# Kernel tuning notes

Hardware: AMD Instinct MI355X
Metric: run time of the kernel (lower is better)

The kernel has to match this reference:

```python
import jax, jax.numpy as jnp
import numpy as np

N = 100000   # nodes
E = 220000   # directed edges (each branch)
H = 128      # hidden_dim
OUT = 1      # output_dim
G = 4096     # num graphs in batch
PE = 5       # laplacian eigenvector PE dims
VOCAB = 28   # atom types


def gcn_conv(x, src, dst, W, b, n):
    # PyG GCNConv: x' = D^-1/2 (A + I) D^-1/2 (X W) + b
    h = x @ W
    deg = jax.ops.segment_sum(jnp.ones(src.shape[0], x.dtype), dst, num_segments=n) + 1.0
    dinv = jax.lax.rsqrt(deg)
    coef = dinv[src] * dinv[dst]                                    # [E]
    agg = jax.ops.segment_sum(h[src] * coef[:, None], dst, num_segments=n)
    agg = agg + h * (dinv * dinv)[:, None]                          # self-loop term
    return agg + b


def gcn2(x, edge_index, W1, b1, W2, b2, n):
    # PyG GCN model, num_layers=2: conv -> relu -> conv
    src, dst = edge_index[0], edge_index[1]
    h = jax.nn.relu(gcn_conv(x, src, dst, W1, b1, n))
    return gcn_conv(h, src, dst, W2, b2, n)


def setup_inputs() -> dict:
    key = jax.random.key(0)
    ks = jax.random.split(key, 16)
    s = 0.1
    return {
        "node_tokens": jax.random.randint(ks[0], (N, 1), 0, VOCAB),
        "pe": jax.random.normal(ks[1], (N, PE), jnp.float32),
        "edge_index": jax.random.randint(ks[2], (2, E), 0, N),
        "vr_edge_index": jax.random.randint(ks[3], (2, E), 0, N),
        "batch": jnp.sort(jax.random.randint(ks[4], (N,), 0, G)),
        "embed_table": jax.random.normal(ks[5], (VOCAB, H), jnp.float32) * s,
        "Wt": jax.random.normal(ks[6], (PE, H), jnp.float32) * s,
        "bt": jnp.zeros((H,), jnp.float32),
        "W1": jax.random.normal(ks[7], (H, H), jnp.float32) * s,
        "b1": jnp.zeros((H,), jnp.float32),
        "W2": jax.random.normal(ks[8], (H, OUT), jnp.float32) * s,
        "b2": jnp.zeros((OUT,), jnp.float32),
        "Wv1": jax.random.normal(ks[9], (H, H), jnp.float32) * s,
        "bv1": jnp.zeros((H,), jnp.float32),
        "Wv2": jax.random.normal(ks[10], (H, OUT), jnp.float32) * s,
        "bv2": jnp.zeros((OUT,), jnp.float32),
    }


def reference(node_tokens, pe, edge_index, vr_edge_index, batch, embed_table,
              Wt, bt, W1, b1, W2, b2, Wv1, bv1, Wv2, bv2):
    # embed_x(data.x.long()).squeeze(1) + lin_trans(pe)
    x = embed_table[node_tokens[:, 0]] + (pe @ Wt + bt)             # [N, H]
    x1 = gcn2(x, edge_index, W1, b1, W2, b2, N)                     # [N, OUT]
    xv = gcn2(x, vr_edge_index, Wv1, bv1, Wv2, bv2, N)              # [N, OUT]
    x1 = x1 + xv
    y_hat = jax.ops.segment_sum(x1, batch, num_segments=G)          # [G, OUT]
    y_hat = jnp.squeeze(y_hat, axis=-1)                             # [G]
    return (y_hat, x)
```

## Files before the change

### kernel.cpp

```cpp
#include <hip/hip_runtime.h>

#define NN 100000
#define NE 220000
#define HD 128
#define NG 4096
#define NPE 5
#define NB_SCAN ((NN + 255) / 256)
#define NBF ((NN + 127) / 128)
#define NBW 128
#define NBZ ((2 * NN + 255) / 256)
#define NBD ((2 * NE + 255) / 256)
#define LDP 136

typedef unsigned int uint;
typedef unsigned short ushort;
typedef __attribute__((ext_vector_type(8))) short bf16x8;
typedef __attribute__((ext_vector_type(4))) float f32x4;

__device__ __forceinline__ float bf2f(uint u16) {
    return __uint_as_float(u16 << 16);
}
__device__ __forceinline__ ushort f2bf(float f) {
    uint u = __float_as_uint(f);
    u += 0x7fffu + ((u >> 16) & 1u);
    return (ushort)(u >> 16);
}

__global__ void k_prep0(const float* __restrict__ W1, const float* __restrict__ Wv1,
                        ushort* __restrict__ Wcat, int* __restrict__ cnt) {
    int b = blockIdx.x;
    if (b < NBW) {
        int t = b * 256 + threadIdx.x;
        int f = t >> 7, k = t & 127;
        const float* W = (f < HD) ? W1 : Wv1;
        Wcat[t] = f2bf(W[k * HD + (f & 127)]);
    } else {
        int t = (b - NBW) * 256 + threadIdx.x;
        if (t < 2 * NN) cnt[t] = 0;
    }
}

__global__ __launch_bounds__(256) void k_front_gemm(
        const int* __restrict__ tok, const float* __restrict__ pe,
        const float* __restrict__ embed, const float* __restrict__ Wtr,
        const float* __restrict__ bt, float* __restrict__ x,
        const ushort* __restrict__ Wcat, ushort* __restrict__ H,
        const int* __restrict__ ei, const int* __restrict__ vei,
        int* __restrict__ cnt) {
    __shared__ ushort As[128 * LDP];
    int b = blockIdx.x;
    if (b < NBF) {
        int tid = threadIdx.x;
        int n0 = b * 128;
        int q = tid & 31;
        int nlb = tid >> 5;
        for (int r = 0; r < 16; ++r) {
            int nl = r * 8 + nlb;
            int n = n0 + nl;
            uint2 pk = {0u, 0u};
            if (n < NN) {
                int t = tok[n];
                float4 acc = ((const float4*)(embed + (size_t)t * HD))[q];
                float4 bv = ((const float4*)bt)[q];
                acc.x += bv.x; acc.y += bv.y; acc.z += bv.z; acc.w += bv.w;
                const float* pen = pe + n * NPE;
#pragma unroll
                for (int k = 0; k < NPE; ++k) {
                    float p = pen[k];
                    float4 wv = ((const float4*)(Wtr + k * HD))[q];
                    acc.x += p * wv.x; acc.y += p * wv.y;
                    acc.z += p * wv.z; acc.w += p * wv.w;
                }
                ((float4*)x)[n * 32 + q] = acc;
                pk.x = (uint)f2bf(acc.x) | ((uint)f2bf(acc.y) << 16);
                pk.y = (uint)f2bf(acc.z) | ((uint)f2bf(acc.w) << 16);
            }
            *(uint2*)&As[nl * LDP + q * 4] = pk;
        }
        __syncthreads();
        int w = tid >> 6, lane = tid & 63;
        int m = lane & 15, quad = lane >> 4;
#pragma unroll
        for (int fh = 0; fh < 2; ++fh) {
            const ushort* Wg = Wcat + (size_t)fh * 128 * 128;
            f32x4 acc[2][8] = {};
#pragma unroll
            for (int kc = 0; kc < 4; ++kc) {
                int k0 = kc * 32 + quad * 8;
                bf16x8 xf[2];
#pragma unroll
                for (int nt = 0; nt < 2; ++nt)
                    xf[nt] = *(const bf16x8*)&As[((w * 2 + nt) * 16 + m) * LDP + k0];
#pragma unroll
                for (int ft = 0; ft < 8; ++ft) {
                    bf16x8 wf = *(const bf16x8*)&Wg[(ft * 16 + m) * 128 + k0];
#pragma unroll
                    for (int nt = 0; nt < 2; ++nt)
                        acc[nt][ft] = __builtin_amdgcn_mfma_f32_16x16x32_bf16(
                            wf, xf[nt], acc[nt][ft], 0, 0, 0);
                }
            }
#pragma unroll
            for (int nt = 0; nt < 2; ++nt) {
                int n = n0 + (w * 2 + nt) * 16 + m;
                if (n >= NN) continue;
#pragma unroll
                for (int ft = 0; ft < 8; ++ft) {
                    f32x4 a = acc[nt][ft];
                    uint2 pk;
                    pk.x = (uint)f2bf(a[0]) | ((uint)f2bf(a[1]) << 16);
                    pk.y = (uint)f2bf(a[2]) | ((uint)f2bf(a[3]) << 16);
                    *(uint2*)&H[(size_t)n * 256 + fh * 128 + ft * 16 + quad * 4] = pk;
                }
            }
        }
    } else {
        int t = (b - NBF) * 256 + threadIdx.x;
        if (t < 2 * NE) {
            int br = t >= NE;
            int e = t - br * NE;
            const int* S = br ? vei : ei;
            atomicAdd(&cnt[br * NN + S[NE + e]], 1);
        }
    }
}

__global__ void k_scan1(const int* __restrict__ cnt, int* __restrict__ off,
                        int* __restrict__ bsum, float* __restrict__ dinv,
                        float* __restrict__ y) {
    __shared__ int s[256];
    int tid = threadIdx.x;
    int gid = blockIdx.x * 256 + tid;
    if (gid < NG) y[gid] = 0.f;
    int br = blockIdx.x / NB_SCAN;
    int blk = blockIdx.x % NB_SCAN;
    int i = blk * 256 + tid;
    int v = (i < NN) ? cnt[br * NN + i] : 0;
    if (i < NN) dinv[br * NN + i] = rsqrtf((float)v + 1.0f);
    s[tid] = v;
    __syncthreads();
    for (int d = 1; d < 256; d <<= 1) {
        int t = (tid >= d) ? s[tid - d] : 0;
        __syncthreads();
        s[tid] += t;
        __syncthreads();
    }
    if (i < NN) off[br * NN + i] = s[tid] - v;
    if (tid == 255) bsum[br * 512 + blk] = s[255];
}

__global__ void k_scan2(int* __restrict__ bsum) {
    __shared__ int s[512];
    int br = blockIdx.x;
    int tid = threadIdx.x;
    int v = (tid < NB_SCAN) ? bsum[br * 512 + tid] : 0;
    s[tid] = v;
    __syncthreads();
    for (int d = 1; d < 512; d <<= 1) {
        int t = (tid >= d) ? s[tid - d] : 0;
        __syncthreads();
        s[tid] += t;
        __syncthreads();
    }
    if (tid < NB_SCAN) bsum[br * 512 + tid] = s[tid] - v;
}

__global__ void k_scan3(const int* __restrict__ off, const int* __restrict__ bsum,
                        const int* __restrict__ cnt, int2* __restrict__ off2,
                        int* __restrict__ cur) {
    int br = blockIdx.x / NB_SCAN;
    int blk = blockIdx.x % NB_SCAN;
    int i = blk * 256 + threadIdx.x;
    if (i < NN) {
        int o = off[br * NN + i] + bsum[br * 512 + blk];
        int2 pr;
        pr.x = o;
        pr.y = o + cnt[br * NN + i];
        off2[br * NN + i] = pr;
        cur[br * NN + i] = o;
    }
}

__global__ void k_scatter(const int* __restrict__ ei, const int* __restrict__ vei,
                          const float* __restrict__ dinv, int* __restrict__ cur,
                          int2* __restrict__ ent) {
    int t = blockIdx.x * blockDim.x + threadIdx.x;
    if (t >= 2 * NE) return;
    int br = t >= NE;
    int e = t - br * NE;
    const int* S = br ? vei : ei;
    int s = S[e], d = S[NE + e];
    int pos = atomicAdd(&cur[br * NN + d], 1);
    int2 rec;
    rec.x = s;
    rec.y = __float_as_int(dinv[br * NN + s] * dinv[br * NN + d]);
    ent[br * NE + pos] = rec;
}

__global__ void k_gather_ep(const ushort* __restrict__ H, const float* __restrict__ dinv,
                            const int2* __restrict__ off2,
                            const int2* __restrict__ ent,
                            const float* __restrict__ b1, const float* __restrict__ bv1,
                            const float* __restrict__ W2, const float* __restrict__ Wv2,
                            float* __restrict__ z) {
    int wid = threadIdx.x >> 6;
    int lane = threadIdx.x & 63;
    int half = lane >> 5;
    int l = lane & 31;
    int task = blockIdx.x * 8 + wid * 2 + half;
    int br = task >= NN;
    int n = task - br * NN;

    const int2* en = ent + br * NE;
    size_t hoff = (size_t)br * 128;

    float dv = dinv[br * NN + n];
    uint2 u = *(const uint2*)(H + (size_t)n * 256 + hoff + l * 4);
    float c = dv * dv;
    float a0 = bf2f(u.x & 0xffffu) * c, a1 = bf2f(u.x >> 16) * c;
    float a2 = bf2f(u.y & 0xffffu) * c, a3 = bf2f(u.y >> 16) * c;

    int2 pr = off2[br * NN + n];
    int p0 = pr.x, p1 = pr.y;
    for (int p = p0; p < p1; p += 4) {
        int2 e0 = en[p], e1 = en[p + 1], e2 = en[p + 2], e3 = en[p + 3];
        int s0 = e0.x;
        int s1 = (p + 1 < p1) ? e1.x : n;
        int s2 = (p + 2 < p1) ? e2.x : n;
        int s3 = (p + 3 < p1) ? e3.x : n;
        float c0 = __int_as_float(e0.y);
        float c1 = (p + 1 < p1) ? __int_as_float(e1.y) : 0.f;
        float c2 = (p + 2 < p1) ? __int_as_float(e2.y) : 0.f;
        float c3 = (p + 3 < p1) ? __int_as_float(e3.y) : 0.f;
        uint2 v0 = *(const uint2*)(H + (size_t)s0 * 256 + hoff + l * 4);
        uint2 v1 = *(const uint2*)(H + (size_t)s1 * 256 + hoff + l * 4);
        uint2 v2 = *(const uint2*)(H + (size_t)s2 * 256 + hoff + l * 4);
        uint2 v3 = *(const uint2*)(H + (size_t)s3 * 256 + hoff + l * 4);
        a0 += bf2f(v0.x & 0xffffu) * c0; a1 += bf2f(v0.x >> 16) * c0;
        a2 += bf2f(v0.y & 0xffffu) * c0; a3 += bf2f(v0.y >> 16) * c0;
        a0 += bf2f(v1.x & 0xffffu) * c1; a1 += bf2f(v1.x >> 16) * c1;
        a2 += bf2f(v1.y & 0xffffu) * c1; a3 += bf2f(v1.y >> 16) * c1;
        a0 += bf2f(v2.x & 0xffffu) * c2; a1 += bf2f(v2.x >> 16) * c2;
        a2 += bf2f(v2.y & 0xffffu) * c2; a3 += bf2f(v2.y >> 16) * c2;
        a0 += bf2f(v3.x & 0xffffu) * c3; a1 += bf2f(v3.x >> 16) * c3;
        a2 += bf2f(v3.y & 0xffffu) * c3; a3 += bf2f(v3.y >> 16) * c3;
    }

    const float* bb = br ? bv1 : b1;
    const float* ww = br ? Wv2 : W2;
    float4 b4 = *(const float4*)&bb[l * 4];
    float4 w4 = *(const float4*)&ww[l * 4];
    float part = fmaxf(a0 + b4.x, 0.f) * w4.x + fmaxf(a1 + b4.y, 0.f) * w4.y
               + fmaxf(a2 + b4.z, 0.f) * w4.z + fmaxf(a3 + b4.w, 0.f) * w4.w;
#pragma unroll
    for (int o = 16; o > 0; o >>= 1) part += __shfl_down(part, o, 32);
    if (l == 0) z[br * NN + n] = part;
}

__global__ void k_final2(const float* __restrict__ z, const float* __restrict__ dinv,
                         const int2* __restrict__ off2,
                         const int2* __restrict__ ent,
                         const float* __restrict__ b2, const float* __restrict__ bv2,
                         const int* __restrict__ batch, float* __restrict__ y) {
    __shared__ float ybuf[256];
    __shared__ int gbase_s;
    int br = blockIdx.x >= NB_SCAN;
    int nb = blockIdx.x - br * NB_SCAN;
    int tid = threadIdx.x;
    ybuf[tid] = 0.f;
    if (tid == 0) gbase_s = batch[nb * 256];
    __syncthreads();
    int gbase = gbase_s;
    int n = nb * 256 + tid;
    if (n < NN) {
        const int2* en = ent + br * NE;
        float dv = dinv[br * NN + n];
        float acc = z[br * NN + n] * dv * dv;
        int2 pr = off2[br * NN + n];
        int p1 = pr.y;
        for (int p = pr.x; p < p1; p += 4) {
            int2 e0 = en[p], e1 = en[p + 1], e2 = en[p + 2], e3 = en[p + 3];
            int s0 = e0.x;
            int s1 = (p + 1 < p1) ? e1.x : n;
            int s2 = (p + 2 < p1) ? e2.x : n;
            int s3 = (p + 3 < p1) ? e3.x : n;
            float c0 = __int_as_float(e0.y);
            float c1 = (p + 1 < p1) ? __int_as_float(e1.y) : 0.f;
            float c2 = (p + 2 < p1) ? __int_as_float(e2.y) : 0.f;
            float c3 = (p + 3 < p1) ? __int_as_float(e3.y) : 0.f;
            acc += c0 * z[br * NN + s0] + c1 * z[br * NN + s1]
                 + c2 * z[br * NN + s2] + c3 * z[br * NN + s3];
        }
        acc += br ? bv2[0] : b2[0];
        int gi = batch[n] - gbase;
        if (gi < 256) atomicAdd(&ybuf[gi], acc);
        else atomicAdd(&y[batch[n]], acc);
    }
    __syncthreads();
    float v = ybuf[tid];
    if (v != 0.f) atomicAdd(&y[gbase + tid], v);
}

extern "C" void kernel_launch(void* const* d_in, const int* in_sizes, int n_in,
                              void* d_out, int out_size, void* d_ws, size_t ws_size,
                              hipStream_t stream) {
    const int*   tok   = (const int*)d_in[0];
    const float* pe    = (const float*)d_in[1];
    const int*   ei    = (const int*)d_in[2];
    const int*   vei   = (const int*)d_in[3];
    const int*   batch = (const int*)d_in[4];
    const float* embed = (const float*)d_in[5];
    const float* Wtr   = (const float*)d_in[6];
    const float* bt    = (const float*)d_in[7];
    const float* W1    = (const float*)d_in[8];
    const float* b1    = (const float*)d_in[9];
    const float* W2    = (const float*)d_in[10];
    const float* b2    = (const float*)d_in[11];
    const float* Wv1   = (const float*)d_in[12];
    const float* bv1   = (const float*)d_in[13];
    const float* Wv2   = (const float*)d_in[14];
    const float* bv2   = (const float*)d_in[15];

    float* y = (float*)d_out;
    float* x = y + NG;

    char* w = (char*)d_ws;
    ushort* H    = (ushort*)w;               w += (size_t)NN * 256 * 2;
    ushort* Wcat = (ushort*)w;               w += 256 * 128 * 2;
    float*  dinv = (float*)w;                w += 2 * NN * 4;
    float*  z    = (float*)w;                w += 2 * NN * 4;
    int*    cnt  = (int*)w;                  w += 2 * NN * 4;
    int*    off  = (int*)w;                  w += 2 * NN * 4;
    int*    cur  = (int*)w;                  w += 2 * NN * 4;
    int2*   off2 = (int2*)w;                 w += (size_t)2 * NN * 8;
    int2*   ent  = (int2*)w;                 w += (size_t)(2 * NE + 8) * 8;
    int*    bsum = (int*)w;                  w += 2 * 512 * 4;

    k_prep0<<<NBW + NBZ, 256, 0, stream>>>(W1, Wv1, Wcat, cnt);
    k_front_gemm<<<NBF + NBD, 256, 0, stream>>>(tok, pe, embed, Wtr, bt, x,
                                                Wcat, H, ei, vei, cnt);
    k_scan1<<<2 * NB_SCAN, 256, 0, stream>>>(cnt, off, bsum, dinv, y);
    k_scan2<<<2, 512, 0, stream>>>(bsum);
    k_scan3<<<2 * NB_SCAN, 256, 0, stream>>>(off, bsum, cnt, off2, cur);
    k_scatter<<<NBD, 256, 0, stream>>>(ei, vei, dinv, cur, ent);
    k_gather_ep<<<2 * NN / 8, 256, 0, stream>>>(H, dinv, off2, ent,
                                                b1, bv1, W2, Wv2, z);
    k_final2<<<2 * NB_SCAN, 256, 0, stream>>>(z, dinv, off2, ent,
                                              b2, bv2, batch, y);
}
```

Baseline: 243.7 us.

## Split fused front-end/GEMM into elementwise embed kernel and separate bf16 GEMM

Splits the fused embedding+GEMM kernel into two. An elementwise kernel computes x (and a bf16 copy) with one thread per float4, and a separate GEMM kernel launches one block per node tile per branch half. The bias is also pre-folded into a small embedding table. The aim is more parallelism: the old fused kernel ran few blocks, and each did serial embedding work followed by two GEMM halves. In exchange it adds an extra kernel launch and a bf16 round trip of x through global memory.

```diff
diff --git a/kernel.cpp b/kernel.cpp
--- a/kernel.cpp
+++ b/kernel.cpp
@@ -6,9 +6,11 @@
 #define NG 4096
 #define NPE 5
 #define NB_SCAN ((NN + 255) / 256)
+#define NBX4 ((NN * HD / 4) / 256)
 #define NBF ((NN + 127) / 128)
 #define NBW 128
 #define NBZ ((2 * NN + 255) / 256)
+#define NBE2 14
 #define NBD ((2 * NE + 255) / 256)
 #define LDP 136
 
@@ -27,100 +29,108 @@
 }
 
 __global__ void k_prep0(const float* __restrict__ W1, const float* __restrict__ Wv1,
-                        ushort* __restrict__ Wcat, int* __restrict__ cnt) {
+                        const float* __restrict__ embed, const float* __restrict__ bt,
+                        ushort* __restrict__ Wcat, int* __restrict__ cnt,
+                        float* __restrict__ embed2) {
     int b = blockIdx.x;
     if (b < NBW) {
         int t = b * 256 + threadIdx.x;
         int f = t >> 7, k = t & 127;
         const float* W = (f < HD) ? W1 : Wv1;
         Wcat[t] = f2bf(W[k * HD + (f & 127)]);
-    } else {
+    } else if (b < NBW + NBZ) {
         int t = (b - NBW) * 256 + threadIdx.x;
         if (t < 2 * NN) cnt[t] = 0;
-    }
-}
-
-__global__ __launch_bounds__(256) void k_front_gemm(
-        const int* __restrict__ tok, const float* __restrict__ pe,
-        const float* __restrict__ embed, const float* __restrict__ Wtr,
-        const float* __restrict__ bt, float* __restrict__ x,
-        const ushort* __restrict__ Wcat, ushort* __restrict__ H,
-        const int* __restrict__ ei, const int* __restrict__ vei,
-        int* __restrict__ cnt) {
-    __shared__ ushort As[128 * LDP];
+    } else {
+        int t = (b - NBW - NBZ) * 256 + threadIdx.x;
+        if (t < 28 * 128) embed2[t] = embed[t] + bt[t & 127];
+    }
+}
+
+__global__ void k_front(const int* __restrict__ tok, const float* __restrict__ pe,
+                        const float* __restrict__ embed2, const float* __restrict__ Wtr,
+                        float* __restrict__ x, ushort* __restrict__ xb,
+                        const int* __restrict__ ei, const int* __restrict__ vei,
+                        int* __restrict__ cnt) {
     int b = blockIdx.x;
-    if (b < NBF) {
-        int tid = threadIdx.x;
-        int n0 = b * 128;
-        int q = tid & 31;
-        int nlb = tid >> 5;
-        for (int r = 0; r < 16; ++r) {
-            int nl = r * 8 + nlb;
-            int n = n0 + nl;
-            uint2 pk = {0u, 0u};
-            if (n < NN) {
-                int t = tok[n];
-                float4 acc = ((const float4*)(embed + (size_t)t * HD))[q];
-                float4 bv = ((const float4*)bt)[q];
-                acc.x += bv.x; acc.y += bv.y; acc.z += bv.z; acc.w += bv.w;
-                const float* pen = pe + n * NPE;
-#pragma unroll
-                for (int k = 0; k < NPE; ++k) {
-                    float p = pen[k];
-                    float4 wv = ((const float4*)(Wtr + k * HD))[q];
-                    acc.x += p * wv.x; acc.y += p * wv.y;
-                    acc.z += p * wv.z; acc.w += p * wv.w;
-                }
-                ((float4*)x)[n * 32 + q] = acc;
-                pk.x = (uint)f2bf(acc.x) | ((uint)f2bf(acc.y) << 16);
-                pk.y = (uint)f2bf(acc.z) | ((uint)f2bf(acc.w) << 16);
-            }
-            *(uint2*)&As[nl * LDP + q * 4] = pk;
-        }
-        __syncthreads();
-        int w = tid >> 6, lane = tid & 63;
-        int m = lane & 15, quad = lane >> 4;
-#pragma unroll
-        for (int fh = 0; fh < 2; ++fh) {
-            const ushort* Wg = Wcat + (size_t)fh * 128 * 128;
-            f32x4 acc[2][8] = {};
-#pragma unroll
-            for (int kc = 0; kc < 4; ++kc) {
-                int k0 = kc * 32 + quad * 8;
-                bf16x8 xf[2];
-#pragma unroll
-                for (int nt = 0; nt < 2; ++nt)
-                    xf[nt] = *(const bf16x8*)&As[((w * 2 + nt) * 16 + m) * LDP + k0];
-#pragma unroll
-                for (int ft = 0; ft < 8; ++ft) {
-                    bf16x8 wf = *(const bf16x8*)&Wg[(ft * 16 + m) * 128 + k0];
-#pragma unroll
-                    for (int nt = 0; nt < 2; ++nt)
-                        acc[nt][ft] = __builtin_amdgcn_mfma_f32_16x16x32_bf16(
-                            wf, xf[nt], acc[nt][ft], 0, 0, 0);
-                }
-            }
-#pragma unroll
-            for (int nt = 0; nt < 2; ++nt) {
-                int n = n0 + (w * 2 + nt) * 16 + m;
-                if (n >= NN) continue;
-#pragma unroll
-                for (int ft = 0; ft < 8; ++ft) {
-                    f32x4 a = acc[nt][ft];
-                    uint2 pk;
-                    pk.x = (uint)f2bf(a[0]) | ((uint)f2bf(a[1]) << 16);
-                    pk.y = (uint)f2bf(a[2]) | ((uint)f2bf(a[3]) << 16);
-                    *(uint2*)&H[(size_t)n * 256 + fh * 128 + ft * 16 + quad * 4] = pk;
-                }
-            }
-        }
+    if (b < NBX4) {
+        int idx = b * 256 + threadIdx.x;
+        int n = idx >> 5, q = idx & 31;
+        int t = tok[n];
+        float4 acc = ((const float4*)(embed2 + (size_t)t * HD))[q];
+        const float* pen = pe + n * NPE;
+#pragma unroll
+        for (int k = 0; k < NPE; ++k) {
+            float p = pen[k];
+            float4 wv = ((const float4*)(Wtr + k * HD))[q];
+            acc.x += p * wv.x; acc.y += p * wv.y;
+            acc.z += p * wv.z; acc.w += p * wv.w;
+        }
+        ((float4*)x)[idx] = acc;
+        uint2 pk;
+        pk.x = (uint)f2bf(acc.x) | ((uint)f2bf(acc.y) << 16);
+        pk.y = (uint)f2bf(acc.z) | ((uint)f2bf(acc.w) << 16);
+        ((uint2*)xb)[idx] = pk;
     } else {
-        int t = (b - NBF) * 256 + threadIdx.x;
+        int t = (b - NBX4) * 256 + threadIdx.x;
         if (t < 2 * NE) {
             int br = t >= NE;
             int e = t - br * NE;
             const int* S = br ? vei : ei;
             atomicAdd(&cnt[br * NN + S[NE + e]], 1);
+        }
+    }
+}
+
+__global__ __launch_bounds__(256) void k_gemm(const ushort* __restrict__ xb,
+                                              const ushort* __restrict__ Wt,
+                                              ushort* __restrict__ H) {
+    __shared__ ushort As[128 * LDP];
+    int bi = blockIdx.x;
+    int fh = bi >= NBF;
+    int n0 = (bi - fh * NBF) * 128;
+    int tid = threadIdx.x;
+    {
+        uint4* dst = (uint4*)As;
+        for (int i = tid; i < 2048; i += 256) {
+            int n = n0 + (i >> 4);
+            uint4 v = {0u, 0u, 0u, 0u};
+            if (n < NN) v = ((const uint4*)(xb + (size_t)n * HD))[i & 15];
+            dst[(i >> 4) * 17 + (i & 15)] = v;
+        }
+    }
+    __syncthreads();
+    int w = tid >> 6, lane = tid & 63;
+    int m = lane & 15, quad = lane >> 4;
+    const ushort* Wg = Wt + (size_t)fh * 128 * 128;
+    f32x4 acc[2][8] = {};
+#pragma unroll
+    for (int kc = 0; kc < 4; ++kc) {
+        int k0 = kc * 32 + quad * 8;
+        bf16x8 xf[2];
+#pragma unroll
+        for (int nt = 0; nt < 2; ++nt)
+            xf[nt] = *(const bf16x8*)&As[((w * 2 + nt) * 16 + m) * LDP + k0];
+#pragma unroll
+        for (int ft = 0; ft < 8; ++ft) {
+            bf16x8 wf = *(const bf16x8*)&Wg[(ft * 16 + m) * 128 + k0];
+#pragma unroll
+            for (int nt = 0; nt < 2; ++nt)
+                acc[nt][ft] = __builtin_amdgcn_mfma_f32_16x16x32_bf16(
+                    wf, xf[nt], acc[nt][ft], 0, 0, 0);
+        }
+    }
+#pragma unroll
+    for (int nt = 0; nt < 2; ++nt) {
+        int n = n0 + (w * 2 + nt) * 16 + m;
+        if (n >= NN) continue;
+#pragma unroll
+        for (int ft = 0; ft < 8; ++ft) {
+            f32x4 a = acc[nt][ft];
+            uint2 pk;
+            pk.x = (uint)f2bf(a[0]) | ((uint)f2bf(a[1]) << 16);
+            pk.y = (uint)f2bf(a[2]) | ((uint)f2bf(a[3]) << 16);
+            *(uint2*)&H[(size_t)n * 256 + fh * 128 + ft * 16 + quad * 4] = pk;
         }
     }
 }
@@ -325,8 +335,10 @@
     float* x = y + NG;
 
     char* w = (char*)d_ws;
+    ushort* xb   = (ushort*)w;               w += (size_t)NN * HD * 2;
     ushort* H    = (ushort*)w;               w += (size_t)NN * 256 * 2;
     ushort* Wcat = (ushort*)w;               w += 256 * 128 * 2;
+    float*  emb2 = (float*)w;                w += 28 * 128 * 4;
     float*  dinv = (float*)w;                w += 2 * NN * 4;
     float*  z    = (float*)w;                w += 2 * NN * 4;
     int*    cnt  = (int*)w;                  w += 2 * NN * 4;
@@ -336,9 +348,9 @@
     int2*   ent  = (int2*)w;                 w += (size_t)(2 * NE + 8) * 8;
     int*    bsum = (int*)w;                  w += 2 * 512 * 4;
 
-    k_prep0<<<NBW + NBZ, 256, 0, stream>>>(W1, Wv1, Wcat, cnt);
-    k_front_gemm<<<NBF + NBD, 256, 0, stream>>>(tok, pe, embed, Wtr, bt, x,
-                                                Wcat, H, ei, vei, cnt);
+    k_prep0<<<NBW + NBZ + NBE2, 256, 0, stream>>>(W1, Wv1, embed, bt, Wcat, cnt, emb2);
+    k_front<<<NBX4 + NBD, 256, 0, stream>>>(tok, pe, emb2, Wtr, x, xb, ei, vei, cnt);
+    k_gemm<<<2 * NBF, 256, 0, stream>>>(xb, Wcat, H);
     k_scan1<<<2 * NB_SCAN, 256, 0, stream>>>(cnt, off, bsum, dinv, y);
     k_scan2<<<2, 512, 0, stream>>>(bsum);
     k_scan3<<<2 * NB_SCAN, 256, 0, stream>>>(off, bsum, cnt, off2, cur);
```

Measured after the change: 255.5 us. 4.8% more time.
